# Kernel tuning notes

Hardware: AMD Instinct MI355X
Metric: run time of the kernel (lower is better)

The kernel has to match this reference:

```python
import jax, jax.numpy as jnp
import numpy as np

N = 100000  # nodes (== in_feats, one-hot id features)
E = 3200000  # edges
D = 64       # out_feats == review_feat dim


def setup_inputs() -> dict:
    key = jax.random.key(0)
    k = jax.random.split(key, 7)
    weight = jax.random.normal(k[0], (N, D), dtype=jnp.float32) * 0.05
    ps_w = jax.random.normal(k[1], (1, D), dtype=jnp.float32) * 0.1
    review_feat = jax.random.normal(k[2], (E, D), dtype=jnp.float32)
    cj = jax.random.uniform(k[3], (N, 1), dtype=jnp.float32)
    ci = jax.random.uniform(k[4], (N, 1), dtype=jnp.float32)
    src = jax.random.randint(k[5], (E,), 0, N, dtype=jnp.int32)
    dst = jax.random.randint(k[6], (E,), 0, N, dtype=jnp.int32)
    return {"weight": weight, "ps_w": ps_w, "review_feat": review_feat,
            "cj": cj, "ci": ci, "src": src, "dst": dst}


def reference(weight, ps_w, review_feat, cj, ci, src, dst):
    # feat = dot_or_identity(None, weight) = weight; dropout_rate=0 -> identity
    feat = weight * cj  # [N, D], degree-normalized src features
    # edge gate: sigmoid(Linear(review_feat)) -> [E, 1]
    pa = jax.nn.sigmoid(review_feat @ ps_w.T)  # [E, 1]
    # message = pa * src_h, then segment-sum to dst (fn.sum)
    msg = pa * feat[src]  # [E, D]
    h = jax.ops.segment_sum(msg, dst, num_segments=weight.shape[0])  # [N, D]
    return h * ci
```

## Files before the change

### kernel.cpp

```cpp
#include <hip/hip_runtime.h>
#include <hip/hip_fp16.h>


#define SCAN_TILE    2048
#define SCAN_THREADS 512
#define HIST_BLOCKS  256
#define GATE_BLOCKS  2048
#define WCJ_BLOCKS   512

__global__ __launch_bounds__(256) void kZ_zero(
    unsigned* __restrict__ deg, unsigned* __restrict__ done, int n)
{
    const int i = blockIdx.x * 256 + threadIdx.x;
    if (i < n) deg[i] = 0u;
    if (i == 0) *done = 0u;
}

__global__ __launch_bounds__(256) void kM_hist_gate(
    const float* __restrict__ review_feat,
    const float* __restrict__ ps_w,
    const int*   __restrict__ dst,
    float*       __restrict__ scale,
    unsigned*    __restrict__ rank,
    unsigned*    __restrict__ deg,
    int E)
{
    if (blockIdx.x < HIST_BLOCKS) {
        const long long gsz = (long long)HIST_BLOCKS * 256;
        const long long t0  = (long long)blockIdx.x * 256 + threadIdx.x;
        for (long long b = t0; b < E; b += gsz * 4) {
            long long e[4];
            int d[4];
            #pragma unroll
            for (int u = 0; u < 4; ++u) {
                e[u] = b + u * gsz;
                d[u] = (e[u] < E) ? dst[e[u]] : 0;
            }
            unsigned r[4];
            #pragma unroll
            for (int u = 0; u < 4; ++u)
                if (e[u] < E) r[u] = atomicAdd(&deg[d[u]], 1u);
            #pragma unroll
            for (int u = 0; u < 4; ++u)
                if (e[u] < E) rank[e[u]] = r[u];
        }
        return;
    }

    const int bid   = blockIdx.x - HIST_BLOCKS;
    const int lane  = threadIdx.x & 63;
    const int wib   = threadIdx.x >> 6;
    const int group = lane >> 4;
    const int sub   = lane & 15;
    const float4 pw = *reinterpret_cast<const float4*>(ps_w + sub * 4);

    const long long nwaves = (long long)GATE_BLOCKS * 4;
    for (long long w = (long long)bid * 4 + wib; w * 16 < E; w += nwaves) {
        const long long ebase = w * 16;
        float4 rv[4];
        #pragma unroll
        for (int u = 0; u < 4; ++u) {
            const long long e = ebase + u * 4 + group;
            rv[u] = (e < E) ? *reinterpret_cast<const float4*>(review_feat + e * 64 + sub * 4)
                            : make_float4(0.f, 0.f, 0.f, 0.f);
        }
        float x[4];
        #pragma unroll
        for (int u = 0; u < 4; ++u) {
            float t = rv[u].x * pw.x + rv[u].y * pw.y + rv[u].z * pw.z + rv[u].w * pw.w;
            t += __shfl_xor(t, 1);
            t += __shfl_xor(t, 2);
            t += __shfl_xor(t, 4);
            t += __shfl_xor(t, 8);
            x[u] = t;
        }
        if (sub == 0) {
            #pragma unroll
            for (int u = 0; u < 4; ++u) {
                const long long e = ebase + u * 4 + group;
                if (e < E) scale[e] = 1.f / (1.f + __expf(-x[u]));
            }
        }
    }
}

__global__ __launch_bounds__(SCAN_THREADS) void k3_scan_onepass(
    const unsigned* __restrict__ deg,
    unsigned*       __restrict__ offs,
    unsigned*       __restrict__ tileagg,
    unsigned*       __restrict__ done,
    int N, int ntiles)
{
    __shared__ unsigned lds[SCAN_TILE];
    __shared__ unsigned sums[SCAN_THREADS];
    __shared__ unsigned sh_prefix;
    const int t = threadIdx.x;
    const int b = blockIdx.x;
    const int base = b * SCAN_TILE;

    #pragma unroll
    for (int i = 0; i < SCAN_TILE / SCAN_THREADS; ++i) {
        const int idx = base + t + i * SCAN_THREADS;
        lds[t + i * SCAN_THREADS] = (idx < N) ? deg[idx] : 0u;
    }
    __syncthreads();

    unsigned v[SCAN_TILE / SCAN_THREADS];
    unsigned s = 0;
    #pragma unroll
    for (int i = 0; i < SCAN_TILE / SCAN_THREADS; ++i) {
        v[i] = lds[(SCAN_TILE / SCAN_THREADS) * t + i];
        s += v[i];
    }
    sums[t] = s;
    __syncthreads();
    for (int off = 1; off < SCAN_THREADS; off <<= 1) {
        const unsigned x = (t >= off) ? sums[t - off] : 0u;
        __syncthreads();
        sums[t] += x;
        __syncthreads();
    }
    unsigned run = sums[t] - s;
    #pragma unroll
    for (int i = 0; i < SCAN_TILE / SCAN_THREADS; ++i) {
        lds[(SCAN_TILE / SCAN_THREADS) * t + i] = run;
        run += v[i];
    }
    __syncthreads();

    const unsigned agg = sums[SCAN_THREADS - 1];
    if (t == 0) {
        atomicExch(&tileagg[b], agg);
        __threadfence();
        atomicAdd(done, 1u);
        while (atomicAdd(done, 0u) < (unsigned)ntiles) { }
        unsigned p = 0;
        for (int i = 0; i < b; ++i) p += atomicAdd(&tileagg[i], 0u);
        sh_prefix = p;
        if (b == ntiles - 1) offs[N] = p + agg;
    }
    __syncthreads();

    const unsigned pfx = sh_prefix;
    #pragma unroll
    for (int i = 0; i < SCAN_TILE / SCAN_THREADS; ++i) {
        const int idx = base + t + i * SCAN_THREADS;
        if (idx < N) offs[idx] = lds[t + i * SCAN_THREADS] + pfx;
    }
}

__global__ __launch_bounds__(256) void k4_scatter_wcj(
    const int*      __restrict__ src,
    const int*      __restrict__ dst,
    const float*    __restrict__ scale,
    const unsigned* __restrict__ rank,
    const unsigned* __restrict__ offs,
    int2*           __restrict__ pairs,
    const float*    __restrict__ weight,
    const float*    __restrict__ cj,
    __half*         __restrict__ wcj,
    int E, int N)
{
    if (blockIdx.x < WCJ_BLOCKS) {
        const long long tid = (long long)blockIdx.x * 256 + threadIdx.x;
        const long long nthreads = (long long)WCJ_BLOCKS * 256;
        const long long nq = (long long)N * 8;
        for (long long i = tid; i < nq; i += nthreads) {
            const int n = (int)(i >> 3);
            const float4 w0 = reinterpret_cast<const float4*>(weight)[i * 2];
            const float4 w1 = reinterpret_cast<const float4*>(weight)[i * 2 + 1];
            const float c = cj[n];
            const unsigned r0 = (unsigned)__half_as_ushort(__float2half(w0.x * c))
                              | ((unsigned)__half_as_ushort(__float2half(w0.y * c)) << 16);
            const unsigned r1 = (unsigned)__half_as_ushort(__float2half(w0.z * c))
                              | ((unsigned)__half_as_ushort(__float2half(w0.w * c)) << 16);
            const unsigned r2 = (unsigned)__half_as_ushort(__float2half(w1.x * c))
                              | ((unsigned)__half_as_ushort(__float2half(w1.y * c)) << 16);
            const unsigned r3 = (unsigned)__half_as_ushort(__float2half(w1.z * c))
                              | ((unsigned)__half_as_ushort(__float2half(w1.w * c)) << 16);
            reinterpret_cast<uint4*>(wcj)[i] = make_uint4(r0, r1, r2, r3);
        }
        return;
    }

    const long long gsz = (long long)(gridDim.x - WCJ_BLOCKS) * 256;
    const long long t0  = (long long)(blockIdx.x - WCJ_BLOCKS) * 256 + threadIdx.x;

    long long e[8];
    int s[8], d[8];
    float sc[8];
    unsigned r[8];
    #pragma unroll
    for (int u = 0; u < 8; ++u) {
        e[u] = t0 + u * gsz;
        const bool ok = e[u] < E;
        s[u]  = ok ? src[e[u]]   : 0;
        d[u]  = ok ? dst[e[u]]   : 0;
        sc[u] = ok ? scale[e[u]] : 0.f;
        r[u]  = ok ? rank[e[u]]  : 0u;
    }
    unsigned o[8];
    #pragma unroll
    for (int u = 0; u < 8; ++u)
        o[u] = (e[u] < E) ? offs[d[u]] : 0u;
    #pragma unroll
    for (int u = 0; u < 8; ++u)
        if (e[u] < E) pairs[o[u] + r[u]] = make_int2(s[u], __float_as_int(sc[u]));
}

__global__ __launch_bounds__(256, 4) void k5_gather(
    const __half*   __restrict__ wcj,
    const float*    __restrict__ ci,
    const unsigned* __restrict__ offs,
    const int2*     __restrict__ pairs,
    float*          __restrict__ out,
    int N)
{
    const int lane  = threadIdx.x & 63;
    const int wib   = threadIdx.x >> 6;
    const int group = lane >> 4;
    const int sub   = lane & 15;

    const long long n = ((long long)blockIdx.x * 4 + wib) * 4 + group;
    const bool valid = (n < N);

    unsigned start = 0, cnt = 0;
    if (valid) { start = offs[n]; cnt = offs[n + 1] - start; }

    int2 p = make_int2(0, 0);
    if (sub < cnt) p = pairs[start + sub];

    float4 acc = make_float4(0.f, 0.f, 0.f, 0.f);
    for (unsigned k0 = 0; __any((int)(k0 < cnt)); k0 += 16) {
        int2 pn = make_int2(0, 0);
        const unsigned nk = k0 + 16;
        if (nk + sub < cnt) pn = pairs[start + nk + sub];

        int m = (int)cnt - (int)k0;
        if (m > 16) m = 16;
        #pragma unroll 8
        for (int j = 0; j < m; ++j) {
            const int   s  = __shfl(p.x, (group << 4) + j);
            const float sc = __int_as_float(__shfl(p.y, (group << 4) + j));
            const uint2 raw = *reinterpret_cast<const uint2*>(
                wcj + (long long)s * 64 + sub * 4);
            acc.x += sc * __half2float(__ushort_as_half((unsigned short)(raw.x & 0xffffu)));
            acc.y += sc * __half2float(__ushort_as_half((unsigned short)(raw.x >> 16)));
            acc.z += sc * __half2float(__ushort_as_half((unsigned short)(raw.y & 0xffffu)));
            acc.w += sc * __half2float(__ushort_as_half((unsigned short)(raw.y >> 16)));
        }
        p = pn;
    }
    if (valid) {
        const float c = ci[n];
        *reinterpret_cast<float4*>(out + n * 64 + sub * 4) =
            make_float4(acc.x * c, acc.y * c, acc.z * c, acc.w * c);
    }
}

extern "C" void kernel_launch(void* const* d_in, const int* in_sizes, int n_in,
                              void* d_out, int out_size, void* d_ws, size_t ws_size,
                              hipStream_t stream) {
    const float* weight      = (const float*)d_in[0];
    const float* ps_w        = (const float*)d_in[1];
    const float* review_feat = (const float*)d_in[2];
    const float* cj          = (const float*)d_in[3];
    const float* ci          = (const float*)d_in[4];
    const int*   src         = (const int*)d_in[5];
    const int*   dst         = (const int*)d_in[6];
    float*       out         = (float*)d_out;

    const int N = in_sizes[3];
    const int E = in_sizes[5];
    const int ntiles = (N + SCAN_TILE - 1) / SCAN_TILE;

    size_t off = 0;
    auto take = [&](size_t bytes) { size_t o = off; off = (off + bytes + 255) & ~(size_t)255; return o; };
    const size_t pairs_o   = take((size_t)E * 8);
    const size_t scale_o   = take((size_t)E * 4);
    const size_t rank_o    = take((size_t)E * 4);
    const size_t wcj_o     = take((size_t)N * 64 * 2);
    const size_t deg_o     = take((size_t)N * 4);
    const size_t offs_o    = take(((size_t)N + 1) * 4);
    const size_t tileagg_o = take((size_t)ntiles * 4);
    const size_t done_o    = take(4);

    char* base = (char*)d_ws;
    int2*     pairs   = (int2*)    (base + pairs_o);
    float*    scale   = (float*)   (base + scale_o);
    unsigned* rank    = (unsigned*)(base + rank_o);
    __half*   wcj     = (__half*)  (base + wcj_o);
    unsigned* deg     = (unsigned*)(base + deg_o);
    unsigned* offs    = (unsigned*)(base + offs_o);
    unsigned* tileagg = (unsigned*)(base + tileagg_o);
    unsigned* done    = (unsigned*)(base + done_o);

    kZ_zero<<<(N + 255) / 256, 256, 0, stream>>>(deg, done, N);
    kM_hist_gate<<<HIST_BLOCKS + GATE_BLOCKS, 256, 0, stream>>>(
        review_feat, ps_w, dst, scale, rank, deg, E);
    k3_scan_onepass<<<ntiles, SCAN_THREADS, 0, stream>>>(deg, offs, tileagg, done,
                                                         N, ntiles);
    const int scatterBlocks = (int)(((long long)E + 8LL * 256 - 1) / (8LL * 256));
    k4_scatter_wcj<<<WCJ_BLOCKS + scatterBlocks, 256, 0, stream>>>(
        src, dst, scale, rank, offs, pairs, weight, cj, wcj, E, N);
    const int blocksD = (N + 15) / 16;
    k5_gather<<<blocksD, 256, 0, stream>>>(wcj, ci, offs, pairs, out, N);
}
```

Measured before the change: 384.5 us.

## Fold degree scan into histogram kernel via grid barrier, add nontemporal gate loads

The separate scan kernel is removed. The first ntiles histogram blocks now wait on a global counter until all histogram blocks finish, then run the tile scan in place with 256 threads per block. The review_feat loads and the gate stores now use nontemporal builtins to reduce cache pollution. This saves one kernel launch, but it depends on all 256 histogram blocks being co-resident while they spin, and the spinning scan blocks hold CU slots that the gate blocks could use.

```diff
diff --git a/kernel.cpp b/kernel.cpp
--- a/kernel.cpp
+++ b/kernel.cpp
@@ -3,46 +3,119 @@
 
 
 #define SCAN_TILE    2048
-#define SCAN_THREADS 512
 #define HIST_BLOCKS  256
 #define GATE_BLOCKS  2048
 #define WCJ_BLOCKS   512
 
+typedef float f32x4 __attribute__((ext_vector_type(4)));
+
 __global__ __launch_bounds__(256) void kZ_zero(
-    unsigned* __restrict__ deg, unsigned* __restrict__ done, int n)
+    unsigned* __restrict__ deg, unsigned* __restrict__ done1,
+    unsigned* __restrict__ done2, int n)
 {
     const int i = blockIdx.x * 256 + threadIdx.x;
     if (i < n) deg[i] = 0u;
-    if (i == 0) *done = 0u;
-}
-
-__global__ __launch_bounds__(256) void kM_hist_gate(
+    if (i == 0) { *done1 = 0u; *done2 = 0u; }
+}
+
+__global__ __launch_bounds__(256) void kM_hist_scan_gate(
     const float* __restrict__ review_feat,
     const float* __restrict__ ps_w,
     const int*   __restrict__ dst,
     float*       __restrict__ scale,
     unsigned*    __restrict__ rank,
     unsigned*    __restrict__ deg,
-    int E)
+    unsigned*    __restrict__ offs,
+    unsigned*    __restrict__ tileagg,
+    unsigned*    __restrict__ done1,
+    unsigned*    __restrict__ done2,
+    int E, int N, int ntiles)
 {
+    __shared__ unsigned lds[SCAN_TILE];
+    __shared__ unsigned sums[256];
+    __shared__ unsigned sh_prefix;
+
     if (blockIdx.x < HIST_BLOCKS) {
-        const long long gsz = (long long)HIST_BLOCKS * 256;
-        const long long t0  = (long long)blockIdx.x * 256 + threadIdx.x;
-        for (long long b = t0; b < E; b += gsz * 4) {
-            long long e[4];
-            int d[4];
-            #pragma unroll
-            for (int u = 0; u < 4; ++u) {
-                e[u] = b + u * gsz;
-                d[u] = (e[u] < E) ? dst[e[u]] : 0;
+        {
+            const long long gsz = (long long)HIST_BLOCKS * 256;
+            const long long t0  = (long long)blockIdx.x * 256 + threadIdx.x;
+            for (long long b = t0; b < E; b += gsz * 4) {
+                long long e[4];
+                int d[4];
+                #pragma unroll
+                for (int u = 0; u < 4; ++u) {
+                    e[u] = b + u * gsz;
+                    d[u] = (e[u] < E) ? dst[e[u]] : 0;
+                }
+                unsigned r[4];
+                #pragma unroll
+                for (int u = 0; u < 4; ++u)
+                    if (e[u] < E) r[u] = atomicAdd(&deg[d[u]], 1u);
+                #pragma unroll
+                for (int u = 0; u < 4; ++u)
+                    if (e[u] < E) rank[e[u]] = r[u];
             }
-            unsigned r[4];
-            #pragma unroll
-            for (int u = 0; u < 4; ++u)
-                if (e[u] < E) r[u] = atomicAdd(&deg[d[u]], 1u);
-            #pragma unroll
-            for (int u = 0; u < 4; ++u)
-                if (e[u] < E) rank[e[u]] = r[u];
+        }
+        __syncthreads();
+        __threadfence();
+        if (threadIdx.x == 0) atomicAdd(done1, 1u);
+        if (blockIdx.x >= (unsigned)ntiles) return;
+
+        if (threadIdx.x == 0) {
+            while (atomicAdd(done1, 0u) < (unsigned)HIST_BLOCKS) { }
+        }
+        __syncthreads();
+
+        const int t = threadIdx.x;
+        const int b = blockIdx.x;
+        const int base = b * SCAN_TILE;
+        #pragma unroll
+        for (int i = 0; i < SCAN_TILE / 256; ++i) {
+            const int idx = base + t + i * 256;
+            lds[t + i * 256] = (idx < N) ? deg[idx] : 0u;
+        }
+        __syncthreads();
+        unsigned v[SCAN_TILE / 256];
+        unsigned s = 0;
+        #pragma unroll
+        for (int i = 0; i < SCAN_TILE / 256; ++i) {
+            v[i] = lds[(SCAN_TILE / 256) * t + i];
+            s += v[i];
+        }
+        sums[t] = s;
+        __syncthreads();
+        for (int off = 1; off < 256; off <<= 1) {
+            const unsigned x = (t >= off) ? sums[t - off] : 0u;
+            __syncthreads();
+            sums[t] += x;
+            __syncthreads();
+        }
+        unsigned run = sums[t] - s;
+        #pragma unroll
+        for (int i = 0; i < SCAN_TILE / 256; ++i) {
+            lds[(SCAN_TILE / 256) * t + i] = run;
+            run += v[i];
+        }
+        __syncthreads();
+
+        const unsigned agg = sums[255];
+        if (t == 0) {
+            atomicExch(&tileagg[b], agg);
+            __threadfence();
+            atomicAdd(done2, 1u);
+            while (atomicAdd(done2, 0u) < (unsigned)ntiles) { }
+            unsigned p = 0;
+            for (int i = 0; i < b; ++i) p += atomicAdd(&tileagg[i], 0u);
+            sh_prefix = p;
+            if (b == ntiles - 1) offs[N] = p + agg;
+        }
+        __syncthreads();
+
+        const unsigned pfx = sh_prefix;
+        #pragma unroll
+        for (int i = 0; i < SCAN_TILE / 256; ++i) {
+            const int idx = base + t + i * 256;
+            if (idx < N) offs[idx] = lds[t + i * 256] + pfx;
         }
         return;
     }
@@ -57,12 +130,16 @@
     const long long nwaves = (long long)GATE_BLOCKS * 4;
     for (long long w = (long long)bid * 4 + wib; w * 16 < E; w += nwaves) {
         const long long ebase = w * 16;
-        float4 rv[4];
+        f32x4 rv[4];
         #pragma unroll
         for (int u = 0; u < 4; ++u) {
             const long long e = ebase + u * 4 + group;
-            rv[u] = (e < E) ? *reinterpret_cast<const float4*>(review_feat + e * 64 + sub * 4)
-                            : make_float4(0.f, 0.f, 0.f, 0.f);
+            if (e < E) {
+                rv[u] = __builtin_nontemporal_load(
+                    reinterpret_cast<const f32x4*>(review_feat + e * 64 + sub * 4));
+            } else {
+                rv[u] = (f32x4){0.f, 0.f, 0.f, 0.f};
+            }
         }
         float x[4];
         #pragma unroll
@@ -78,74 +155,12 @@
             #pragma unroll
             for (int u = 0; u < 4; ++u) {
                 const long long e = ebase + u * 4 + group;
-                if (e < E) scale[e] = 1.f / (1.f + __expf(-x[u]));
+                if (e < E) {
+                    const float g = 1.f / (1.f + __expf(-x[u]));
+                    __builtin_nontemporal_store(g, scale + e);
+                }
             }
         }
-    }
-}
-
-__global__ __launch_bounds__(SCAN_THREADS) void k3_scan_onepass(
-    const unsigned* __restrict__ deg,
-    unsigned*       __restrict__ offs,
-    unsigned*       __restrict__ tileagg,
-    unsigned*       __restrict__ done,
-    int N, int ntiles)
-{
-    __shared__ unsigned lds[SCAN_TILE];
-    __shared__ unsigned sums[SCAN_THREADS];
-    __shared__ unsigned sh_prefix;
-    const int t = threadIdx.x;
-    const int b = blockIdx.x;
-    const int base = b * SCAN_TILE;
-
-    #pragma unroll
-    for (int i = 0; i < SCAN_TILE / SCAN_THREADS; ++i) {
-        const int idx = base + t + i * SCAN_THREADS;
-        lds[t + i * SCAN_THREADS] = (idx < N) ? deg[idx] : 0u;
-    }
-    __syncthreads();
-
-    unsigned v[SCAN_TILE / SCAN_THREADS];
-    unsigned s = 0;
-    #pragma unroll
-    for (int i = 0; i < SCAN_TILE / SCAN_THREADS; ++i) {
-        v[i] = lds[(SCAN_TILE / SCAN_THREADS) * t + i];
-        s += v[i];
-    }
-    sums[t] = s;
-    __syncthreads();
-    for (int off = 1; off < SCAN_THREADS; off <<= 1) {
-        const unsigned x = (t >= off) ? sums[t - off] : 0u;
-        __syncthreads();
-        sums[t] += x;
-        __syncthreads();
-    }
-    unsigned run = sums[t] - s;
-    #pragma unroll
-    for (int i = 0; i < SCAN_TILE / SCAN_THREADS; ++i) {
-        lds[(SCAN_TILE / SCAN_THREADS) * t + i] = run;
-        run += v[i];
-    }
-    __syncthreads();
-
-    const unsigned agg = sums[SCAN_THREADS - 1];
-    if (t == 0) {
-        atomicExch(&tileagg[b], agg);
-        __threadfence();
-        atomicAdd(done, 1u);
-        while (atomicAdd(done, 0u) < (unsigned)ntiles) { }
-        unsigned p = 0;
-        for (int i = 0; i < b; ++i) p += atomicAdd(&tileagg[i], 0u);
-        sh_prefix = p;
-        if (b == ntiles - 1) offs[N] = p + agg;
-    }
-    __syncthreads();
-
-    const unsigned pfx = sh_prefix;
-    #pragma unroll
-    for (int i = 0; i < SCAN_TILE / SCAN_THREADS; ++i) {
-        const int idx = base + t + i * SCAN_THREADS;
-        if (idx < N) offs[idx] = lds[t + i * SCAN_THREADS] + pfx;
     }
 }
 
@@ -283,7 +298,8 @@
     const size_t deg_o     = take((size_t)N * 4);
     const size_t offs_o    = take(((size_t)N + 1) * 4);
     const size_t tileagg_o = take((size_t)ntiles * 4);
-    const size_t done_o    = take(4);
+    const size_t done1_o   = take(4);
+    const size_t done2_o   = take(4);
 
     char* base = (char*)d_ws;
     int2*     pairs   = (int2*)    (base + pairs_o);
@@ -293,13 +309,13 @@
     unsigned* deg     = (unsigned*)(base + deg_o);
     unsigned* offs    = (unsigned*)(base + offs_o);
     unsigned* tileagg = (unsigned*)(base + tileagg_o);
-    unsigned* done    = (unsigned*)(base + done_o);
-
-    kZ_zero<<<(N + 255) / 256, 256, 0, stream>>>(deg, done, N);
-    kM_hist_gate<<<HIST_BLOCKS + GATE_BLOCKS, 256, 0, stream>>>(
-        review_feat, ps_w, dst, scale, rank, deg, E);
-    k3_scan_onepass<<<ntiles, SCAN_THREADS, 0, stream>>>(deg, offs, tileagg, done,
-                                                         N, ntiles);
+    unsigned* done1   = (unsigned*)(base + done1_o);
+    unsigned* done2   = (unsigned*)(base + done2_o);
+
+    kZ_zero<<<(N + 255) / 256, 256, 0, stream>>>(deg, done1, done2, N);
+    kM_hist_scan_gate<<<HIST_BLOCKS + GATE_BLOCKS, 256, 0, stream>>>(
+        review_feat, ps_w, dst, scale, rank, deg, offs, tileagg, done1, done2,
+        E, N, ntiles);
     const int scatterBlocks = (int)(((long long)E + 8LL * 256 - 1) / (8LL * 256));
     k4_scatter_wcj<<<WCJ_BLOCKS + scatterBlocks, 256, 0, stream>>>(
         src, dst, scale, rank, offs, pairs, weight, cj, wcj, E, N);
```

Result: slower. 427.4 us (+11.1%).
